# Kernel optimization log

Hardware: AMD Instinct MI355X
Metric: run time of the kernel (lower is better)

Reference implementation:

```python
import jax, jax.numpy as jnp
import numpy as np

B, T, C, D, H, NT, ND = 256, 64, 4880, 128, 1024, 101, 10


def setup_inputs() -> dict:
    key = jax.random.key(0)
    ks = jax.random.split(key, 12)
    Hs = (jax.random.uniform(ks[0], (B, C, T)) < 0.005).astype(jnp.float32)  # multi-hot codes per visit
    timestamps = jnp.arange(NT, dtype=jnp.float32) * 0.1  # grid matches rk4 step_size=0.1
    last_idx = jax.random.randint(ks[1], (B,), 0, NT)
    llm_idx = jax.random.randint(ks[2], (B, ND), 0, C)
    eps = jax.random.normal(ks[3], (B, H), dtype=jnp.float32)
    s = lambda k, sh, fan: (jax.random.normal(k, sh, dtype=jnp.float32) / np.float32(np.sqrt(fan)))
    return dict(
        Hs=Hs, timestamps=timestamps, last_idx=last_idx, llm_idx=llm_idx, eps=eps,
        emb_table=s(ks[4], (C, D), D),
        gru_Wih=s(ks[5], (3 * H, D), D),
        gru_Whh=s(ks[6], (3 * H, H), H),
        gru_bih=jnp.zeros((3 * H,), jnp.float32),
        gru_bhh=jnp.zeros((3 * H,), jnp.float32),
        attn_w=s(ks[7], (H,), H),
        fc_mu_W=s(ks[8], (H, H), H), fc_mu_b=jnp.zeros((H,), jnp.float32),
        fc_var_W=s(ks[9], (H, H), H), fc_var_b=jnp.zeros((H,), jnp.float32),
        ode_Whz=s(ks[10], (H, H), H),
        ode_Whn=s(ks[11], (H, H), H),
    )


def reference(Hs, timestamps, last_idx, llm_idx, eps, emb_table, gru_Wih, gru_Whh,
              gru_bih, gru_bhh, attn_w, fc_mu_W, fc_mu_b, fc_var_W, fc_var_b,
              ode_Whz, ode_Whn):
    # ---- Encoder (vectorized over patients) ----
    visit_emb = jnp.einsum('bct,cd->btd', Hs, emb_table)  # H.T @ X per patient: [B,T,D]
    gi = visit_emb @ gru_Wih.T + gru_bih                  # precompute input gates [B,T,3H]

    def gru_step(h, gi_t):
        gh = h @ gru_Whh.T + gru_bhh
        i_r, i_z, i_n = jnp.split(gi_t, 3, axis=-1)
        h_r, h_z, h_n = jnp.split(gh, 3, axis=-1)
        r = jax.nn.sigmoid(i_r + h_r)
        z = jax.nn.sigmoid(i_z + h_z)
        n = jnp.tanh(i_n + r * h_n)
        h_new = (1.0 - z) * n + z * h
        return h_new, h_new

    h0 = jnp.zeros((Hs.shape[0], gru_Whh.shape[1]), dtype=visit_emb.dtype)
    _, hs = jax.lax.scan(gru_step, h0, jnp.swapaxes(gi, 0, 1))  # [T,B,H]
    hs = jnp.swapaxes(hs, 0, 1)                                  # [B,T,H]

    alpha = jax.nn.softmax(hs @ attn_w, axis=-1)                 # [B,T]
    henc = jnp.einsum('bt,bth->bh', alpha, hs)                   # [B,H]

    # ---- VAE reparameterization ----
    mu = henc @ fc_mu_W.T + fc_mu_b
    log_var = henc @ fc_var_W.T + fc_var_b
    z0 = mu + jnp.exp(0.5 * log_var) * eps                       # [B,H]

    # ---- GRU-ODE integrated with RK4 (one step per grid interval, dt=0.1) ----
    def f(h):
        zz = jax.nn.sigmoid(h @ ode_Whz.T)
        nn_ = jnp.tanh((zz * h) @ ode_Whn.T)
        return (1.0 - zz) * (nn_ - h)

    def rk4(h, dt):
        k1 = f(h)
        k2 = f(h + 0.5 * dt * k1)
        k3 = f(h + 0.5 * dt * k2)
        k4 = f(h + dt * k3)
        hn = h + (dt / 6.0) * (k1 + 2.0 * k2 + 2.0 * k3 + k4)
        return hn, hn

    dts = timestamps[1:] - timestamps[:-1]
    _, traj = jax.lax.scan(rk4, z0, dts)                         # [NT-1,B,H]
    pred_z = jnp.concatenate([z0[None], traj], axis=0)           # [NT,B,H]
    pred_z = jnp.swapaxes(pred_z, 0, 1)                          # [B,NT,H]

    # ---- per-patient last-visit state + LLM diagnosis mask ----
    last_visit_emb = pred_z[jnp.arange(pred_z.shape[0]), last_idx]  # [B,H]
    mask = jnp.zeros((Hs.shape[0], C), jnp.float32).at[
        jnp.arange(Hs.shape[0])[:, None], llm_idx].set(1.0)          # [B,4880]
    return last_visit_emb, mask
```

## Files before the change

### kernel.cpp

```cpp
#include <hip/hip_runtime.h>
#include <hip/hip_bf16.h>

#define DEVI __device__ __forceinline__

namespace {

constexpr int nB = 256, nT = 64, nC = 4880, nD = 128, nH = 1024, nNT = 101, nND = 10;

typedef __attribute__((ext_vector_type(8))) short bfrag;
typedef __attribute__((ext_vector_type(4))) float ffrag;
typedef __attribute__((ext_vector_type(4))) unsigned int uvec4;

DEVI ffrag mfma16(bfrag a, bfrag b, ffrag c) {
  return __builtin_amdgcn_mfma_f32_16x16x32_bf16(a, b, c, 0, 0, 0);
}

DEVI unsigned short f2b(float x) {
  __hip_bfloat16 h = __float2bfloat16(x);
  return *reinterpret_cast<unsigned short*>(&h);
}
DEVI float b2f(unsigned short u) {
  __hip_bfloat16 h;
  *reinterpret_cast<unsigned short*>(&h) = u;
  return __bfloat162float(h);
}
DEVI float sigm(float x) { return 1.f / (1.f + expf(-x)); }

template<int NS>
DEVI void mm_stream(ffrag (&acc)[NS],
                    const unsigned short* __restrict__ A, int lda, int K,
                    const unsigned short* const (&Wp)[NS], int ldw,
                    int m0, int n0, int tid, int lane, int mq, int nq,
                    unsigned short* As, unsigned short* Ws) {
  const int r = tid >> 3, blk = tid & 7;
  const int wrOff = (r * 8 + (blk ^ (r & 7))) * 8;
  const int ra = mq * 16 + (lane & 15);
  const int rw = nq * 16 + (lane & 15);
  const int q = lane >> 4;
  const int nc = K >> 6;

  uvec4 va = *(const uvec4*)(A + (size_t)(m0 + r) * lda + blk * 8);
  uvec4 vw[NS];
#pragma unroll
  for (int s = 0; s < NS; ++s)
    vw[s] = *(const uvec4*)(Wp[s] + (size_t)(n0 + r) * ldw + blk * 8);
  *(uvec4*)(As + wrOff) = va;
#pragma unroll
  for (int s = 0; s < NS; ++s) *(uvec4*)(Ws + s * 2048 + wrOff) = vw[s];

  for (int ci = 0; ci < nc; ++ci) {
    __syncthreads();
    const int cur = ci & 1;
    const bool more = (ci + 1) < nc;
    if (more) {
      const int k0 = (ci + 1) << 6;
      va = *(const uvec4*)(A + (size_t)(m0 + r) * lda + k0 + blk * 8);
#pragma unroll
      for (int s = 0; s < NS; ++s)
        vw[s] = *(const uvec4*)(Wp[s] + (size_t)(n0 + r) * ldw + k0 + blk * 8);
    }
    const unsigned short* Ab = As + cur * 2048;
    const unsigned short* Wb = Ws + cur * (NS * 2048);
#pragma unroll
    for (int kk = 0; kk < 2; ++kk) {
      bfrag af = *(const bfrag*)(Ab + (ra * 8 + ((kk * 4 + q) ^ (ra & 7))) * 8);
#pragma unroll
      for (int s = 0; s < NS; ++s) {
        bfrag wf = *(const bfrag*)(Wb + s * 2048 + (rw * 8 + ((kk * 4 + q) ^ (rw & 7))) * 8);
        acc[s] = mfma16(af, wf, acc[s]);
      }
    }
    if (more) {
      const int nx = cur ^ 1;
      *(uvec4*)(As + nx * 2048 + wrOff) = va;
#pragma unroll
      for (int s = 0; s < NS; ++s)
        *(uvec4*)(Ws + nx * (NS * 2048) + s * 2048 + wrOff) = vw[s];
    }
  }
  __syncthreads();
}

__global__ void k_cvt(const float* __restrict__ s, unsigned short* __restrict__ d, int n) {
  int i = blockIdx.x * blockDim.x + threadIdx.x;
  float4 v = ((const float4*)s)[i];
  unsigned int u0 = (unsigned int)f2b(v.x) | ((unsigned int)f2b(v.y) << 16);
  unsigned int u1 = (unsigned int)f2b(v.z) | ((unsigned int)f2b(v.w) << 16);
  ((uint2*)d)[i] = make_uint2(u0, u1);
}

__global__ void k_mask(const int* __restrict__ llm, float* __restrict__ outm) {
  int c = blockIdx.x * 256 + threadIdx.x;
  int b = blockIdx.y;
  if (c >= nC) return;
  const int* lr = llm + b * nND;
  float v = 0.f;
#pragma unroll
  for (int i = 0; i < nND; ++i) v = (lr[i] == c) ? 1.f : v;
  outm[(size_t)b * nC + c] = v;
}

__global__ void k_embed(const float* __restrict__ Hs, const float* __restrict__ emb,
                        unsigned short* __restrict__ ve) {
  __shared__ float tile[4][16][128];
  const int b = blockIdx.x;
  const int tid = threadIdx.x;
  const int w = tid >> 6, lane = tid & 63;
  float* tw = &tile[w][0][0];
  for (int i = lane; i < 16 * 128; i += 64) tw[i] = 0.f;
  const float* hb = Hs + (size_t)b * nC * nT;
  const int tq = w * 16;
  const int tl = lane & 15;
  const int co = lane >> 4;
  for (int cb = 0; cb < nC; cb += 4) {
    const int c = cb + co;
    float v = hb[(size_t)c * nT + tq + tl];
    unsigned long long m = __ballot(v != 0.f);
    while (m) {
      const int p = __ffsll(m) - 1;
      m &= m - 1;
      const int cc = cb + (p >> 4);
      const int tt = p & 15;
      const float vv = __shfl(v, p);
      const float* er = emb + (size_t)cc * nD;
      tile[w][tt][lane]      += vv * er[lane];
      tile[w][tt][lane + 64] += vv * er[lane + 64];
    }
  }
  for (int rr = 0; rr < 16; ++rr) {
    unsigned short* o = ve + ((size_t)b * nT + tq + rr) * nD;
    o[lane]      = f2b(tile[w][rr][lane]);
    o[lane + 64] = f2b(tile[w][rr][lane + 64]);
  }
}

__global__ void k_attn(const unsigned short* __restrict__ hsb,
                       const float* __restrict__ aw,
                       unsigned short* __restrict__ hencb) {
  __shared__ float sc[nT];
  __shared__ float al[nT];
  const int b = blockIdx.x;
  const int tid = threadIdx.x;
  const int w = tid >> 6, lane = tid & 63;
  for (int t = w; t < nT; t += 4) {
    const unsigned short* hr = hsb + ((size_t)b * nT + t) * nH;
    float s = 0.f;
    for (int i = lane; i < nH; i += 64) s += b2f(hr[i]) * aw[i];
#pragma unroll
    for (int o = 32; o > 0; o >>= 1) s += __shfl_xor(s, o);
    if (lane == 0) sc[t] = s;
  }
  __syncthreads();
  if (tid < nT) {
    float v = sc[tid];
    float mx = v;
#pragma unroll
    for (int o = 32; o > 0; o >>= 1) mx = fmaxf(mx, __shfl_xor(mx, o));
    float e = expf(v - mx);
    float su = e;
#pragma unroll
    for (int o = 32; o > 0; o >>= 1) su += __shfl_xor(su, o);
    al[tid] = e / su;
  }
  __syncthreads();
  for (int col = tid; col < nH; col += 256) {
    float a = 0.f;
    for (int t = 0; t < nT; ++t) a += al[t] * b2f(hsb[((size_t)b * nT + t) * nH + col]);
    hencb[(size_t)b * nH + col] = f2b(a);
  }
}

__global__ __launch_bounds__(256) void k_vae(
    const unsigned short* __restrict__ hencb,
    const unsigned short* __restrict__ Wmu, const unsigned short* __restrict__ Wvar,
    const float* __restrict__ bmu, const float* __restrict__ bvar,
    const float* __restrict__ eps,
    float* __restrict__ hf, unsigned short* __restrict__ hb,
    const int* __restrict__ lidx, float* __restrict__ out) {
  __shared__ __align__(16) unsigned short As[2 * 2048];
  __shared__ __align__(16) unsigned short Ws[2 * 2 * 2048];
  const int tid = threadIdx.x, lane = tid & 63, w = tid >> 6;
  const int mq = w & 1, nq = w >> 1;
  const int m0 = blockIdx.x * 32, n0 = blockIdx.y * 32;
  ffrag acc[2] = {};
  const unsigned short* const Wp[2] = {Wmu, Wvar};
  mm_stream<2>(acc, hencb, nH, nH, Wp, nH, m0, n0, tid, lane, mq, nq, As, Ws);
  const int col = n0 + nq * 16 + (lane & 15);
  const int rb = m0 + mq * 16 + ((lane >> 4) << 2);
#pragma unroll
  for (int i = 0; i < 4; ++i) {
    const int row = rb + i;
    const size_t idx = (size_t)row * nH + col;
    const float mu = acc[0][i] + bmu[col];
    const float lv = acc[1][i] + bvar[col];
    const float z0 = mu + expf(0.5f * lv) * eps[idx];
    hf[idx] = z0;
    hb[idx] = f2b(z0);
    if (lidx[row] == 0) out[idx] = z0;
  }
}

DEVI void rb_bar(unsigned* c, unsigned tgt) {
  asm volatile("s_waitcnt vmcnt(0)" ::: "memory");
  __syncthreads();
  if (threadIdx.x == 0) {
    __hip_atomic_fetch_add(c, 1u, __ATOMIC_RELAXED, __HIP_MEMORY_SCOPE_AGENT);
    while (__hip_atomic_load(c, __ATOMIC_RELAXED, __HIP_MEMORY_SCOPE_AGENT) < tgt)
      __builtin_amdgcn_s_sleep(2);
  }
  __syncthreads();
}

DEVI void stageW(const unsigned short* __restrict__ Wg, int n0, int tid,
                 unsigned short* Ws) {
  const int r = tid >> 3, b0 = tid & 7;
  const unsigned short* src = Wg + (size_t)(n0 + r) * nH;
  unsigned short* dst = Ws + r * 1024;
#pragma unroll
  for (int t2 = 0; t2 < 16; ++t2) {
    const int blk = b0 + 8 * t2;
    *(uvec4*)(dst + (blk ^ (r & 7)) * 8) = *(const uvec4*)(src + blk * 8);
  }
}

DEVI void ld8w(uvec4 (&d)[8], const unsigned short* p) {
  asm volatile(
      "global_load_dwordx4 %0, %8, off sc0\n\t"
      "global_load_dwordx4 %1, %8, off offset:64 sc0\n\t"
      "global_load_dwordx4 %2, %8, off offset:128 sc0\n\t"
      "global_load_dwordx4 %3, %8, off offset:192 sc0\n\t"
      "global_load_dwordx4 %4, %8, off offset:256 sc0\n\t"
      "global_load_dwordx4 %5, %8, off offset:320 sc0\n\t"
      "global_load_dwordx4 %6, %8, off offset:384 sc0\n\t"
      "global_load_dwordx4 %7, %8, off offset:448 sc0\n\t"
      "s_waitcnt vmcnt(0)"
      : "=&v"(d[0]), "=&v"(d[1]), "=&v"(d[2]), "=&v"(d[3]),
        "=&v"(d[4]), "=&v"(d[5]), "=&v"(d[6]), "=&v"(d[7])
      : "v"(p)
      : "memory");
}

DEVI ffrag mm_l2(const unsigned short* ag, const unsigned short* wrow,
                 int q, int rx) {
  ffrag a0 = {0.f, 0.f, 0.f, 0.f}, a1 = {0.f, 0.f, 0.f, 0.f};
#pragma unroll
  for (int g = 0; g < 4; ++g) {
    uvec4 A[8];
    ld8w(A, ag + g * 256);
#pragma unroll
    for (int k8 = 0; k8 < 8; k8 += 2) {
      const int kk = g * 8 + k8;
      a0 = mfma16(*(const bfrag*)&A[k8],
                  *(const bfrag*)(wrow + (((kk * 4 + q) ^ rx) * 8)), a0);
      a1 = mfma16(*(const bfrag*)&A[k8 + 1],
                  *(const bfrag*)(wrow + ((((kk + 1) * 4 + q) ^ rx) * 8)), a1);
    }
  }
  return a0 + a1;
}

DEVI void pack_store(const float v[4], unsigned short* pkw, int lane,
                     unsigned short* dst ) {
  const int cl = lane & 15, r0l = (lane >> 4) << 2;
#pragma unroll
  for (int i = 0; i < 4; ++i) pkw[(r0l + i) * 16 + cl] = f2b(v[i]);
  asm volatile("s_waitcnt lgkmcnt(0)" ::: "memory");
  __builtin_amdgcn_sched_barrier(0);
  const int pr = lane >> 2, pc = (lane & 3) << 2;
  *(unsigned long long*)(dst + pr * nH + pc) =
      *(const unsigned long long*)(pkw + pr * 16 + pc);
}

DEVI void pack_store2(const float v[4], unsigned short* pkw, int lane,
                      unsigned short* d1 ,
                      unsigned short* d2 ) {
  const int cl = lane & 15, r0l = (lane >> 4) << 2;
#pragma unroll
  for (int i = 0; i < 4; ++i) pkw[(r0l + i) * 16 + cl] = f2b(v[i]);
  asm volatile("s_waitcnt lgkmcnt(0)" ::: "memory");
  __builtin_amdgcn_sched_barrier(0);
  const int pr = lane >> 2, pc = (lane & 3) << 2;
  const unsigned long long val = *(const unsigned long long*)(pkw + pr * 16 + pc);
  *(unsigned long long*)(d1 + (size_t)pr * nH + pc) = val;
  *(unsigned long long*)(d2 + (size_t)pr * (nT * nH) + pc) = val;
}

__global__ __launch_bounds__(256, 1) void k_gru_persist(
    const unsigned short* __restrict__ Whh_g, const unsigned short* __restrict__ Wih_g,
    const float* __restrict__ bih, const float* __restrict__ bhh,
    const unsigned short* __restrict__ ve,
    unsigned short* hA, unsigned short* hB,
    unsigned short* hsb, unsigned* ctr) {
  __shared__ __align__(16) unsigned short Wr[32 * nH];
  __shared__ __align__(16) unsigned short Wz2[32 * nH];
  __shared__ __align__(16) unsigned short Wi[96 * nD];
  __shared__ __align__(16) unsigned short pk[4][16][16];
  __shared__ unsigned rank_sh;
  const int tid = threadIdx.x, lane = tid & 63, w = tid >> 6;
  const int mq = w & 1, nq = w >> 1;

  unsigned xcd;
  asm volatile("s_getreg_b32 %0, hwreg(HW_REG_XCC_ID)" : "=s"(xcd));
  if (tid == 0)
    rank_sh = __hip_atomic_fetch_add(ctr + 1536 + (xcd & 7) * 16, 1u,
                                     __ATOMIC_RELAXED, __HIP_MEMORY_SCOPE_AGENT);
  __syncthreads();
  const int i = (int)(xcd & 7);
  const int j = (int)(rank_sh & 31);
  const int m0 = i * 32, n0 = j * 32;

  stageW(Whh_g, n0, tid, Wr);
  stageW(Whh_g + (size_t)nH * nH, n0, tid, Wz2);
  for (int idx = tid; idx < 96 * 16; idx += 256) {
    const int r = idx >> 4, blk = idx & 15;
    const int gate = r >> 5, rr2 = r & 31;
    *(uvec4*)(Wi + r * nD + ((blk ^ (r & 7)) * 8)) =
        *(const uvec4*)(Wih_g + ((size_t)gate * nH + n0 + rr2) * nD + blk * 8);
  }

  const int col = n0 + nq * 16 + (lane & 15);
  const int arow = m0 + mq * 16 + (lane & 15);
  const int q = lane >> 4;
  const int rw = nq * 16 + (lane & 15);
  const int rx = rw & 7;
  const unsigned short* wrr = Wr + rw * nH;
  const unsigned short* wzr = Wz2 + rw * nH;
  const unsigned short* wir = Wi + rw * nD;
  const unsigned short* wiz = Wi + (32 + rw) * nD;
  const unsigned short* win = Wi + (64 + rw) * nD;
  const unsigned short* wng = Whh_g + ((size_t)2 * nH + col) * nH + q * 8;
  const unsigned short* aA = hA + (size_t)arow * nH + q * 8;
  const unsigned short* aB = hB + (size_t)arow * nH + q * 8;
  unsigned short* dA = hA + (size_t)(m0 + mq * 16) * nH + n0 + nq * 16;
  unsigned short* dB = hB + (size_t)(m0 + mq * 16) * nH + n0 + nq * 16;
  unsigned short* dh = hsb + (size_t)(m0 + mq * 16) * nT * nH + n0 + nq * 16;
  unsigned short* pkw = &pk[w][0][0];
  const float b_r = bih[col] + bhh[col];
  const float b_z = bih[nH + col] + bhh[nH + col];
  const float bi_n = bih[2 * nH + col];
  const float bh_n = bhh[2 * nH + col];

  float hf_[4] = {0.f, 0.f, 0.f, 0.f};
  unsigned* myc = ctr + 1024 + i * 64;
  unsigned ph = 0;
  __syncthreads();

#pragma unroll 1
  for (int t = 0; t < nT; ++t) {
    const unsigned short* ah = (t & 1) ? aB : aA;
    unsigned short* dst = (t & 1) ? dA : dB;
    ffrag ar = {0.f, 0.f, 0.f, 0.f}, az = {0.f, 0.f, 0.f, 0.f},
          an = {0.f, 0.f, 0.f, 0.f};
#pragma unroll
    for (int g = 0; g < 4; ++g) {
      uvec4 A[8];
      ld8w(A, ah + g * 256);
#pragma unroll
      for (int k8 = 0; k8 < 8; ++k8) {
        const int kk = g * 8 + k8;
        const int wo = ((kk * 4 + q) ^ rx) * 8;
        const bfrag af = *(const bfrag*)&A[k8];
        ar = mfma16(af, *(const bfrag*)(wrr + wo), ar);
        az = mfma16(af, *(const bfrag*)(wzr + wo), az);
        an = mfma16(af, *(const bfrag*)(wng + kk * 32), an);
      }
    }
    ffrag ir = {0.f, 0.f, 0.f, 0.f}, iz = {0.f, 0.f, 0.f, 0.f},
          in_ = {0.f, 0.f, 0.f, 0.f};
    const unsigned short* av = ve + ((size_t)arow * nT + t) * nD + q * 8;
#pragma unroll
    for (int kk = 0; kk < 4; ++kk) {
      const bfrag af = *(const bfrag*)(av + kk * 32);
      const int wo = ((kk * 4 + q) ^ rx) * 8;
      ir = mfma16(af, *(const bfrag*)(wir + wo), ir);
      iz = mfma16(af, *(const bfrag*)(wiz + wo), iz);
      in_ = mfma16(af, *(const bfrag*)(win + wo), in_);
    }
    float hv[4];
#pragma unroll
    for (int ii = 0; ii < 4; ++ii) {
      const float rr2 = sigm(ar[ii] + ir[ii] + b_r);
      const float zv = sigm(az[ii] + iz[ii] + b_z);
      const float nn = tanhf(in_[ii] + bi_n + rr2 * (an[ii] + bh_n));
      const float hn2 = (1.f - zv) * nn + zv * hf_[ii];
      hf_[ii] = hn2;
      hv[ii] = hn2;
    }
    pack_store2(hv, pkw, lane, dst, dh + (size_t)t * nH);
    ph += 32; rb_bar(myc, ph);
  }
}

__global__ __launch_bounds__(256, 1) void k_ode_persist(
    const unsigned short* __restrict__ Wz_g, const unsigned short* __restrict__ Wn_g,
    const float* __restrict__ h0f, unsigned short* xb, unsigned short* gbuf,
    const float* __restrict__ ts, const int* __restrict__ lidx,
    float* __restrict__ out, unsigned* ctr) {
  __shared__ __align__(16) unsigned short Wz[32 * nH];
  __shared__ __align__(16) unsigned short Wn[32 * nH];
  __shared__ __align__(16) unsigned short pk[4][16][16];
  __shared__ unsigned rank_sh;
  const int tid = threadIdx.x, lane = tid & 63, w = tid >> 6;
  const int mq = w & 1, nq = w >> 1;

  unsigned xcd;
  asm volatile("s_getreg_b32 %0, hwreg(HW_REG_XCC_ID)" : "=s"(xcd));
  if (tid == 0)
    rank_sh = __hip_atomic_fetch_add(ctr + 512 + (xcd & 7) * 16, 1u,
                                     __ATOMIC_RELAXED, __HIP_MEMORY_SCOPE_AGENT);
  __syncthreads();
  const int i = (int)(xcd & 7);
  const int j = (int)(rank_sh & 31);
  const int m0 = i * 32, n0 = j * 32;

  stageW(Wz_g, n0, tid, Wz);
  stageW(Wn_g, n0, tid, Wn);

  const int col = n0 + nq * 16 + (lane & 15);
  const int row0 = m0 + mq * 16 + ((lane >> 4) << 2);
  const int arow = m0 + mq * 16 + (lane & 15);
  const int q = lane >> 4;
  const int rw = nq * 16 + (lane & 15);
  const int rx = rw & 7;
  const unsigned short* wzrow = Wz + rw * nH;
  const unsigned short* wnrow = Wn + rw * nH;
  const unsigned short* axb = xb + (size_t)arow * nH + q * 8;
  const unsigned short* agb = gbuf + (size_t)arow * nH + q * 8;
  unsigned short* pkw = &pk[w][0][0];
  unsigned short* gdst = gbuf + (size_t)(m0 + mq * 16) * nH + n0 + nq * 16;
  unsigned short* xdst = xb + (size_t)(m0 + mq * 16) * nH + n0 + nq * 16;

  float hb[4], xv[4], ka[4];
  int lst[4];
#pragma unroll
  for (int ii = 0; ii < 4; ++ii) {
    hb[ii] = h0f[(size_t)(row0 + ii) * nH + col];
    xv[ii] = hb[ii];
    lst[ii] = lidx[row0 + ii];
  }
  unsigned* myc = ctr + i * 64;
  unsigned ph = 0;
  __syncthreads();

  for (int s = 0; s < nNT - 1; ++s) {
    const float dt = ts[s + 1] - ts[s];
#pragma unroll 1
    for (int stg = 0; stg < 4; ++stg) {
      ffrag acc = mm_l2(axb, wzrow, q, rx);
      float zv[4], gv[4];
#pragma unroll
      for (int ii = 0; ii < 4; ++ii) {
        zv[ii] = sigm(acc[ii]);
        gv[ii] = zv[ii] * xv[ii];
      }
      pack_store(gv, pkw, lane, gdst);
      ph += 32; rb_bar(myc, ph);
      acc = mm_l2(agb, wnrow, q, rx);
#pragma unroll
      for (int ii = 0; ii < 4; ++ii) {
        const float nn = tanhf(acc[ii]);
        const float fv = (1.f - zv[ii]) * (nn - xv[ii]);
        if (stg == 0)      { ka[ii] = fv;        xv[ii] = hb[ii] + 0.5f * dt * fv; }
        else if (stg == 1) { ka[ii] += 2.f * fv; xv[ii] = hb[ii] + 0.5f * dt * fv; }
        else if (stg == 2) { ka[ii] += 2.f * fv; xv[ii] = hb[ii] + dt * fv; }
        else {
          const float hn = hb[ii] + (dt * (1.f / 6.f)) * (ka[ii] + fv);
          hb[ii] = hn; xv[ii] = hn;
          if (lst[ii] == s + 1) out[(size_t)(row0 + ii) * nH + col] = hn;
        }
      }
      pack_store(xv, pkw, lane, xdst);
      ph += 32; rb_bar(myc, ph);
    }
  }
}

}

extern "C" void kernel_launch(void* const* d_in, const int* in_sizes, int n_in,
                              void* d_out, int out_size, void* d_ws, size_t ws_size,
                              hipStream_t stream) {
  const float* Hs   = (const float*)d_in[0];
  const float* ts   = (const float*)d_in[1];
  const int*   lidx = (const int*)d_in[2];
  const int*   llm  = (const int*)d_in[3];
  const float* eps  = (const float*)d_in[4];
  const float* emb  = (const float*)d_in[5];
  const float* Wih  = (const float*)d_in[6];
  const float* Whh  = (const float*)d_in[7];
  const float* bih  = (const float*)d_in[8];
  const float* bhh  = (const float*)d_in[9];
  const float* aw   = (const float*)d_in[10];
  const float* Wmu  = (const float*)d_in[11];
  const float* bmu  = (const float*)d_in[12];
  const float* Wvar = (const float*)d_in[13];
  const float* bvar = (const float*)d_in[14];
  const float* Whz  = (const float*)d_in[15];
  const float* Whn  = (const float*)d_in[16];

  float* out_last = (float*)d_out;
  float* out_mask = out_last + (size_t)nB * nH;

  char* p = (char*)d_ws;
  auto alloc = [&](size_t bytes) {
    void* r = p; p += (bytes + 255) & ~(size_t)255; return r;
  };
  unsigned short* Whh_b  = (unsigned short*)alloc((size_t)3 * nH * nH * 2);
  unsigned short* Wih_b  = (unsigned short*)alloc((size_t)3 * nH * nD * 2);
  unsigned short* Wmu_b  = (unsigned short*)alloc((size_t)nH * nH * 2);
  unsigned short* Wvar_b = (unsigned short*)alloc((size_t)nH * nH * 2);
  unsigned short* Whz_b  = (unsigned short*)alloc((size_t)nH * nH * 2);
  unsigned short* Whn_b  = (unsigned short*)alloc((size_t)nH * nH * 2);
  unsigned short* ve_b   = (unsigned short*)alloc((size_t)nB * nT * nD * 2);
  unsigned short* hs_b   = (unsigned short*)alloc((size_t)nB * nT * nH * 2);
  float* h0f             = (float*)alloc((size_t)nB * nH * 4);
  unsigned short* h0b    = (unsigned short*)alloc((size_t)nB * nH * 2);
  unsigned short* h1b    = (unsigned short*)alloc((size_t)nB * nH * 2);
  unsigned short* gb     = (unsigned short*)alloc((size_t)nB * nH * 2);
  unsigned short* hencb  = (unsigned short*)alloc((size_t)nB * nH * 2);
  unsigned* ctr          = (unsigned*)alloc(8192);

  hipMemsetAsync(h0b, 0, (size_t)nB * nH * 2, stream);
  hipMemsetAsync(ctr, 0, 8192, stream);

  auto cvt = [&](const float* s, unsigned short* d, int n) {
    k_cvt<<<n / 1024, 256, 0, stream>>>(s, d, n);
  };
  cvt(Whh, Whh_b, 3 * nH * nH);
  cvt(Wih, Wih_b, 3 * nH * nD);
  cvt(Wmu, Wmu_b, nH * nH);
  cvt(Wvar, Wvar_b, nH * nH);
  cvt(Whz, Whz_b, nH * nH);
  cvt(Whn, Whn_b, nH * nH);

  k_embed<<<nB, 256, 0, stream>>>(Hs, emb, ve_b);
  k_mask<<<dim3((nC + 255) / 256, nB), 256, 0, stream>>>(llm, out_mask);

  k_gru_persist<<<256, 256, 0, stream>>>(Whh_b, Wih_b, bih, bhh, ve_b,
                                         h0b, h1b, hs_b, ctr);

  k_attn<<<nB, 256, 0, stream>>>(hs_b, aw, hencb);
  const dim3 gg(nB / 32, nH / 32);
  k_vae<<<gg, 256, 0, stream>>>(hencb, Wmu_b, Wvar_b, bmu, bvar, eps,
                                h0f, h0b, lidx, out_last);

  k_ode_persist<<<256, 256, 0, stream>>>(Whz_b, Whn_b, h0f, h0b, gb, ts, lidx,
                                         out_last, ctr);
}
```

Measured before the change: 5.392 ms.

## Split ODE row blocks into two independently synchronized halves with split-K waves

The persistent RK4 ODE kernel now divides each block's 32 batch rows into two 16-row groups, each with its own cross-block counter. While one group waits on its barrier, the block computes the other group, which is meant to hide the global barrier latency. The four waves now split the K dimension in halves and reduce partial sums through shared memory rather than splitting M. This adds intra-block syncs and an LDS reduction, leaves half the waves idle during the elementwise update, and makes the counter protocol more complex.

```diff
diff --git a/kernel.cpp b/kernel.cpp
--- a/kernel.cpp
+++ b/kernel.cpp
@@ -211,6 +211,18 @@
   __syncthreads();
 }
 
+DEVI void cp_arrive(unsigned* c) {
+  if (threadIdx.x == 0)
+    __hip_atomic_fetch_add(c, 1u, __ATOMIC_RELAXED, __HIP_MEMORY_SCOPE_AGENT);
+}
+DEVI void cp_wait(unsigned* c, unsigned tgt) {
+  if (threadIdx.x == 0) {
+    while (__hip_atomic_load(c, __ATOMIC_RELAXED, __HIP_MEMORY_SCOPE_AGENT) < tgt)
+      __builtin_amdgcn_s_sleep(2);
+  }
+  __syncthreads();
+}
+
 DEVI void stageW(const unsigned short* __restrict__ Wg, int n0, int tid,
                  unsigned short* Ws) {
   const int r = tid >> 3, b0 = tid & 7;
@@ -259,6 +271,25 @@
   return a0 + a1;
 }
 
+DEVI ffrag mm_half(const unsigned short* ag, const unsigned short* wrow,
+                   int q, int rx, int kq) {
+  ffrag a0 = {0.f, 0.f, 0.f, 0.f}, a1 = {0.f, 0.f, 0.f, 0.f};
+#pragma unroll
+  for (int g = 0; g < 2; ++g) {
+    uvec4 A[8];
+    ld8w(A, ag + kq * 512 + g * 256);
+#pragma unroll
+    for (int k8 = 0; k8 < 8; k8 += 2) {
+      const int kk = kq * 16 + g * 8 + k8;
+      a0 = mfma16(*(const bfrag*)&A[k8],
+                  *(const bfrag*)(wrow + (((kk * 4 + q) ^ rx) * 8)), a0);
+      a1 = mfma16(*(const bfrag*)&A[k8 + 1],
+                  *(const bfrag*)(wrow + ((((kk + 1) * 4 + q) ^ rx) * 8)), a1);
+    }
+  }
+  return a0 + a1;
+}
+
 DEVI void pack_store(const float v[4], unsigned short* pkw, int lane,
                      unsigned short* dst ) {
   const int cl = lane & 15, r0l = (lane >> 4) << 2;
@@ -272,8 +303,7 @@
 }
 
 DEVI void pack_store2(const float v[4], unsigned short* pkw, int lane,
-                      unsigned short* d1 ,
-                      unsigned short* d2 ) {
+                      unsigned short* d1, unsigned short* d2) {
   const int cl = lane & 15, r0l = (lane >> 4) << 2;
 #pragma unroll
   for (int i = 0; i < 4; ++i) pkw[(r0l + i) * 16 + cl] = f2b(v[i]);
@@ -399,80 +429,131 @@
   __shared__ __align__(16) unsigned short Wz[32 * nH];
   __shared__ __align__(16) unsigned short Wn[32 * nH];
   __shared__ __align__(16) unsigned short pk[4][16][16];
+  __shared__ float red[2][16][17];
   __shared__ unsigned rank_sh;
   const int tid = threadIdx.x, lane = tid & 63, w = tid >> 6;
-  const int mq = w & 1, nq = w >> 1;
+  const int kq = w & 1, nq = w >> 1;
 
   unsigned xcd;
   asm volatile("s_getreg_b32 %0, hwreg(HW_REG_XCC_ID)" : "=s"(xcd));
   if (tid == 0)
-    rank_sh = __hip_atomic_fetch_add(ctr + 512 + (xcd & 7) * 16, 1u,
+    rank_sh = __hip_atomic_fetch_add(ctr + 2048 + (xcd & 7) * 16, 1u,
                                      __ATOMIC_RELAXED, __HIP_MEMORY_SCOPE_AGENT);
   __syncthreads();
-  const int i = (int)(xcd & 7);
+  const int ix = (int)(xcd & 7);
   const int j = (int)(rank_sh & 31);
-  const int m0 = i * 32, n0 = j * 32;
+  const int n0 = j * 32;
+  const int rowA = ix * 32, rowB = rowA + 16;
 
   stageW(Wz_g, n0, tid, Wz);
   stageW(Wn_g, n0, tid, Wn);
 
   const int col = n0 + nq * 16 + (lane & 15);
-  const int row0 = m0 + mq * 16 + ((lane >> 4) << 2);
-  const int arow = m0 + mq * 16 + (lane & 15);
   const int q = lane >> 4;
+  const int rl4 = (lane >> 4) << 2;
   const int rw = nq * 16 + (lane & 15);
   const int rx = rw & 7;
   const unsigned short* wzrow = Wz + rw * nH;
   const unsigned short* wnrow = Wn + rw * nH;
-  const unsigned short* axb = xb + (size_t)arow * nH + q * 8;
-  const unsigned short* agb = gbuf + (size_t)arow * nH + q * 8;
+  const unsigned short* axA = xb + (size_t)(rowA + (lane & 15)) * nH + q * 8;
+  const unsigned short* axB = xb + (size_t)(rowB + (lane & 15)) * nH + q * 8;
+  const unsigned short* agA = gbuf + (size_t)(rowA + (lane & 15)) * nH + q * 8;
+  const unsigned short* agB = gbuf + (size_t)(rowB + (lane & 15)) * nH + q * 8;
   unsigned short* pkw = &pk[w][0][0];
-  unsigned short* gdst = gbuf + (size_t)(m0 + mq * 16) * nH + n0 + nq * 16;
-  unsigned short* xdst = xb + (size_t)(m0 + mq * 16) * nH + n0 + nq * 16;
-
-  float hb[4], xv[4], ka[4];
-  int lst[4];
+  unsigned short* gdA = gbuf + (size_t)rowA * nH + n0 + nq * 16;
+  unsigned short* gdB = gbuf + (size_t)rowB * nH + n0 + nq * 16;
+  unsigned short* xdA = xb + (size_t)rowA * nH + n0 + nq * 16;
+  unsigned short* xdB = xb + (size_t)rowB * nH + n0 + nq * 16;
+
+  float hbA[4], xvA[4], kaA[4], zvA[4];
+  float hbB[4], xvB[4], kaB[4], zvB[4];
+  int lstA[4], lstB[4];
+  const int row0A = rowA + rl4, row0B = rowB + rl4;
 #pragma unroll
   for (int ii = 0; ii < 4; ++ii) {
-    hb[ii] = h0f[(size_t)(row0 + ii) * nH + col];
-    xv[ii] = hb[ii];
-    lst[ii] = lidx[row0 + ii];
-  }
-  unsigned* myc = ctr + i * 64;
-  unsigned ph = 0;
-  __syncthreads();
-
-  for (int s = 0; s < nNT - 1; ++s) {
+    hbA[ii] = h0f[(size_t)(row0A + ii) * nH + col];
+    xvA[ii] = hbA[ii];
+    lstA[ii] = lidx[row0A + ii];
+    hbB[ii] = h0f[(size_t)(row0B + ii) * nH + col];
+    xvB[ii] = hbB[ii];
+    lstB[ii] = lidx[row0B + ii];
+  }
+  unsigned* cA = ctr + (ix * 2 + 0) * 64;
+  unsigned* cB = ctr + (ix * 2 + 1) * 64;
+  unsigned base = 0;
+  __syncthreads();
+
+#define MM1_LET(AX, GD, ZV, XV)                                           \
+  {                                                                       \
+    ffrag acc = mm_half(AX, wzrow, q, rx, kq);                            \
+    if (kq == 1) {                                                        \
+      _Pragma("unroll")                                                   \
+      for (int ii = 0; ii < 4; ++ii) red[nq][rl4 + ii][lane & 15] = acc[ii]; \
+    }                                                                     \
+    __syncthreads();                                                      \
+    if (kq == 0) {                                                        \
+      float gv[4];                                                        \
+      _Pragma("unroll")                                                   \
+      for (int ii = 0; ii < 4; ++ii) {                                    \
+        acc[ii] += red[nq][rl4 + ii][lane & 15];                          \
+        ZV[ii] = sigm(acc[ii]);                                           \
+        gv[ii] = ZV[ii] * XV[ii];                                         \
+      }                                                                   \
+      pack_store(gv, pkw, lane, GD);                                      \
+      asm volatile("s_waitcnt vmcnt(0)" ::: "memory");                    \
+    }                                                                     \
+    __syncthreads();                                                      \
+  }
+
+#define MM2_LET(AG, XD, ZV, XV, HB, KA, LST, ROW0)                        \
+  {                                                                       \
+    ffrag acc = mm_half(AG, wnrow, q, rx, kq);                            \
+    if (kq == 1) {                                                        \
+      _Pragma("unroll")                                                   \
+      for (int ii = 0; ii < 4; ++ii) red[nq][rl4 + ii][lane & 15] = acc[ii]; \
+    }                                                                     \
+    __syncthreads();                                                      \
+    if (kq == 0) {                                                        \
+      _Pragma("unroll")                                                   \
+      for (int ii = 0; ii < 4; ++ii) {                                    \
+        acc[ii] += red[nq][rl4 + ii][lane & 15];                          \
+        const float nn = tanhf(acc[ii]);                                  \
+        const float fv = (1.f - ZV[ii]) * (nn - XV[ii]);                  \
+        if (stg == 0)      { KA[ii] = fv;        XV[ii] = HB[ii] + 0.5f * dt * fv; } \
+        else if (stg == 1) { KA[ii] += 2.f * fv; XV[ii] = HB[ii] + 0.5f * dt * fv; } \
+        else if (stg == 2) { KA[ii] += 2.f * fv; XV[ii] = HB[ii] + dt * fv; } \
+        else {                                                            \
+          const float hn = HB[ii] + (dt * (1.f / 6.f)) * (KA[ii] + fv);   \
+          HB[ii] = hn; XV[ii] = hn;                                       \
+          if (LST[ii] == s + 1) out[(size_t)(ROW0 + ii) * nH + col] = hn; \
+        }                                                                 \
+      }                                                                   \
+      pack_store(XV, pkw, lane, XD);                                      \
+      asm volatile("s_waitcnt vmcnt(0)" ::: "memory");                    \
+    }                                                                     \
+    __syncthreads();                                                      \
+  }
+
+#pragma unroll 1
+  for (int p = 0; p < 4 * (nNT - 1); ++p) {
+    const int s = p >> 2, stg = p & 3;
     const float dt = ts[s + 1] - ts[s];
-#pragma unroll 1
-    for (int stg = 0; stg < 4; ++stg) {
-      ffrag acc = mm_l2(axb, wzrow, q, rx);
-      float zv[4], gv[4];
-#pragma unroll
-      for (int ii = 0; ii < 4; ++ii) {
-        zv[ii] = sigm(acc[ii]);
-        gv[ii] = zv[ii] * xv[ii];
-      }
-      pack_store(gv, pkw, lane, gdst);
-      ph += 32; rb_bar(myc, ph);
-      acc = mm_l2(agb, wnrow, q, rx);
-#pragma unroll
-      for (int ii = 0; ii < 4; ++ii) {
-        const float nn = tanhf(acc[ii]);
-        const float fv = (1.f - zv[ii]) * (nn - xv[ii]);
-        if (stg == 0)      { ka[ii] = fv;        xv[ii] = hb[ii] + 0.5f * dt * fv; }
-        else if (stg == 1) { ka[ii] += 2.f * fv; xv[ii] = hb[ii] + 0.5f * dt * fv; }
-        else if (stg == 2) { ka[ii] += 2.f * fv; xv[ii] = hb[ii] + dt * fv; }
-        else {
-          const float hn = hb[ii] + (dt * (1.f / 6.f)) * (ka[ii] + fv);
-          hb[ii] = hn; xv[ii] = hn;
-          if (lst[ii] == s + 1) out[(size_t)(row0 + ii) * nH + col] = hn;
-        }
-      }
-      pack_store(xv, pkw, lane, xdst);
-      ph += 32; rb_bar(myc, ph);
-    }
-  }
+    cp_wait(cA, base);
+    MM1_LET(axA, gdA, zvA, xvA)
+    cp_arrive(cA);
+    cp_wait(cB, base);
+    MM1_LET(axB, gdB, zvB, xvB)
+    cp_arrive(cB);
+    cp_wait(cA, base + 32);
+    MM2_LET(agA, xdA, zvA, xvA, hbA, kaA, lstA, row0A)
+    cp_arrive(cA);
+    cp_wait(cB, base + 32);
+    MM2_LET(agB, xdB, zvB, xvB, hbB, kaB, lstB, row0B)
+    cp_arrive(cB);
+    base += 64;
+  }
+#undef MM1_LET
+#undef MM2_LET
 }
 
 }
@@ -518,10 +599,10 @@
   unsigned short* h1b    = (unsigned short*)alloc((size_t)nB * nH * 2);
   unsigned short* gb     = (unsigned short*)alloc((size_t)nB * nH * 2);
   unsigned short* hencb  = (unsigned short*)alloc((size_t)nB * nH * 2);
-  unsigned* ctr          = (unsigned*)alloc(8192);
+  unsigned* ctr          = (unsigned*)alloc(16384);
 
   hipMemsetAsync(h0b, 0, (size_t)nB * nH * 2, stream);
-  hipMemsetAsync(ctr, 0, 8192, stream);
+  hipMemsetAsync(ctr, 0, 16384, stream);
 
   auto cvt = [&](const float* s, unsigned short* d, int n) {
     k_cvt<<<n / 1024, 256, 0, stream>>>(s, d, n);
```

New measurement: 6.290 ms. +16.6%, slower.
